# Performance work log

Hardware: AMD Instinct MI355X
Metric: run time of the kernel (lower is better)

## Reference

```python
import jax, jax.numpy as jnp
import numpy as np

D = 128  # inputs / head dim

def setup_inputs() -> dict:
    key = jax.random.key(0)
    ks = jax.random.split(key, 7)
    B, S = 4, 4096
    s = 1.0 / np.sqrt(D)
    return {
        "x": jax.random.normal(ks[0], (B, S, D), dtype=jnp.float32),
        "Wq": jax.random.normal(ks[1], (D, D), dtype=jnp.float32) * s,
        "bq": jax.random.normal(ks[2], (D,), dtype=jnp.float32) * s,
        "Wk": jax.random.normal(ks[3], (D, D), dtype=jnp.float32) * s,
        "bk": jax.random.normal(ks[4], (D,), dtype=jnp.float32) * s,
        "Wv": jax.random.normal(ks[5], (D, D), dtype=jnp.float32) * s,
        "bv": jax.random.normal(ks[6], (D,), dtype=jnp.float32) * s,
    }

def reference(x, Wq, bq, Wk, bk, Wv, bv):
    B, S, d = x.shape
    # nn.Linear: y = x @ W^T + b
    q = jnp.einsum('bsd,ed->bse', x, Wq) + bq
    k = jnp.einsum('bsd,ed->bse', x, Wk) + bk
    v = jnp.einsum('bsd,ed->bse', x, Wv) + bv
    scores = jnp.einsum('bse,bte->bst', q, k) / jnp.sqrt(jnp.asarray(d, x.dtype))
    attn = jax.nn.softmax(scores, axis=-1)
    out = jnp.einsum('bst,bte->bse', attn, v)
    return out.reshape(B, S * d)
```

## Files before the change

kernel.cpp:

```cpp
#include <hip/hip_runtime.h>
#include <hip/hip_bf16.h>

typedef __bf16 bf16x8 __attribute__((ext_vector_type(8)));
typedef __bf16 bf16x4 __attribute__((ext_vector_type(4)));
typedef float  f32x4  __attribute__((ext_vector_type(4)));
typedef _Float16 f16x4 __attribute__((ext_vector_type(4)));

#define NB 4
#define SEQ 4096
#define DIM 128

static __device__ __forceinline__ unsigned int bf16bits(__bf16 h) {
    return (unsigned int)__builtin_bit_cast(unsigned short, h);
}

#define GLOAD_LDS16(g, s) __builtin_amdgcn_global_load_lds(                    \
    (const __attribute__((address_space(1))) void*)(g),                        \
    (__attribute__((address_space(3))) void*)(s), 16, 0, 0)

__global__ __launch_bounds__(256) void wconv(
    const float* __restrict__ Wq, const float* __restrict__ Wk,
    const float* __restrict__ Wv,
    __bf16* __restrict__ Wh, __bf16* __restrict__ Wl)
{
    int idx = blockIdx.x * 256 + threadIdx.x;
    int which = idx >> 12;
    int off = (idx & 4095) * 4;
    const float* W = which == 0 ? Wq : (which == 1 ? Wk : Wv);
    float4 v = *(const float4*)(W + off);
    bf16x4 h, lo;
    h[0] = (__bf16)v.x; h[1] = (__bf16)v.y; h[2] = (__bf16)v.z; h[3] = (__bf16)v.w;
    lo[0] = (__bf16)(v.x - (float)h[0]);
    lo[1] = (__bf16)(v.y - (float)h[1]);
    lo[2] = (__bf16)(v.z - (float)h[2]);
    lo[3] = (__bf16)(v.w - (float)h[3]);
    *(bf16x4*)(Wh + which * 16384 + off) = h;
    *(bf16x4*)(Wl + which * 16384 + off) = lo;
}

union QkvSh {
    float  xs[64][132];
    __bf16 vbuf[64][200];
};

__global__ __launch_bounds__(256) void qkv_proj3(
    const float* __restrict__ x,
    const __bf16* __restrict__ Whg, const __bf16* __restrict__ Wlg,
    const float* __restrict__ bq, const float* __restrict__ bk,
    const float* __restrict__ bv,
    __bf16* __restrict__ Q, __bf16* __restrict__ K, __bf16* __restrict__ Vt)
{
    __shared__ QkvSh sh;
    const int t  = threadIdx.x;
    const int w  = t >> 6, l = t & 63, lg = l >> 4, ll = l & 15;
    const int rt = blockIdx.x;
    const int ct0 = blockIdx.y * 12;

    {
        const float4* xsrc = (const float4*)(x + rt * 64 * 128);
        #pragma unroll
        for (int ii = 0; ii < 8; ++ii) {
            int u = t + ii * 256;
            float4 v4 = xsrc[u];
            *(float4*)&sh.xs[u >> 5][(u & 31) * 4] = v4;
        }
    }
    __syncthreads();

    float bfr[3];
    #pragma unroll
    for (int i = 0; i < 3; ++i) {
        int gct = ct0 + w * 3 + i;
        const float* bias = gct < 8 ? bq : (gct < 16 ? bk : bv);
        bfr[i] = bias[(gct & 7) * 16 + ll];
    }

    f32x4 acc[3][4];
    #pragma unroll
    for (int i = 0; i < 3; ++i)
        #pragma unroll
        for (int rf = 0; rf < 4; ++rf) acc[i][rf] = (f32x4){0.f, 0.f, 0.f, 0.f};

    #pragma unroll 1
    for (int kb = 0; kb < 4; ++kb) {
        bf16x8 xh[4], xl[4];
        #pragma unroll
        for (int rf = 0; rf < 4; ++rf) {
            float4 xa = *(const float4*)&sh.xs[rf * 16 + ll][kb * 32 + lg * 8];
            float4 xb = *(const float4*)&sh.xs[rf * 16 + ll][kb * 32 + lg * 8 + 4];
            float xv[8] = {xa.x, xa.y, xa.z, xa.w, xb.x, xb.y, xb.z, xb.w};
            #pragma unroll
            for (int j = 0; j < 8; ++j) {
                __bf16 h = (__bf16)xv[j];
                xh[rf][j] = h;
                xl[rf][j] = (__bf16)(xv[j] - (float)h);
            }
        }
        #pragma unroll
        for (int i = 0; i < 3; ++i) {
            int gct = ct0 + w * 3 + i;
            const __bf16* wb = Whg + (gct >> 3) * 16384 + ((gct & 7) * 16 + ll) * 128 + kb * 32 + lg * 8;
            const __bf16* lb = Wlg + (gct >> 3) * 16384 + ((gct & 7) * 16 + ll) * 128 + kb * 32 + lg * 8;
            bf16x8 wh = *(const bf16x8*)wb;
            bf16x8 wl = *(const bf16x8*)lb;
            #pragma unroll
            for (int rf = 0; rf < 4; ++rf) {
                acc[i][rf] = __builtin_amdgcn_mfma_f32_16x16x32_bf16(xh[rf], wh, acc[i][rf], 0, 0, 0);
                acc[i][rf] = __builtin_amdgcn_mfma_f32_16x16x32_bf16(xh[rf], wl, acc[i][rf], 0, 0, 0);
                acc[i][rf] = __builtin_amdgcn_mfma_f32_16x16x32_bf16(xl[rf], wh, acc[i][rf], 0, 0, 0);
            }
        }
    }

    __syncthreads();
    const float qscale = 0.08838834764831845f;
    #pragma unroll
    for (int i = 0; i < 3; ++i) {
        int gct = ct0 + w * 3 + i;
        float scale = (gct < 8) ? qscale : 1.0f;
        int lct = w * 3 + i;
        #pragma unroll
        for (int rf = 0; rf < 4; ++rf)
            #pragma unroll
            for (int r = 0; r < 4; ++r)
                sh.vbuf[rf * 16 + lg * 4 + r][lct * 16 + ll] =
                    (__bf16)((acc[i][rf][r] + bfr[i]) * scale);
    }
    __syncthreads();

    #pragma unroll 1
    for (int lct = 0; lct < 12; ++lct) {
        int gct = ct0 + lct;
        if (gct < 16) {
            int row = t >> 2, c = (t & 3) * 4;
            __bf16* base = (gct < 8 ? Q : K);
            bf16x4 v4 = *(const bf16x4*)&sh.vbuf[row][lct * 16 + c];
            *(bf16x4*)(base + (rt * 64 + row) * 128 + (gct & 7) * 16 + c) = v4;
        } else {
            int e = (gct - 16) * 16 + (t >> 4);
            int s0 = (t & 15) * 4;
            int bb = rt >> 6, sb = (rt & 63) * 64 + s0;
            bf16x4 v4;
            #pragma unroll
            for (int j = 0; j < 4; ++j) v4[j] = sh.vbuf[s0 + j][lct * 16 + (t >> 4)];
            *(bf16x4*)(Vt + bb * (128 * 4096) + e * 4096 + sb) = v4;
        }
    }
}

__global__ __launch_bounds__(256, 2) void attn_fwd(
    const __bf16* __restrict__ Qg,
    const __bf16* __restrict__ Kg,
    const __bf16* __restrict__ Vt,
    _Float16* __restrict__ Op, float* __restrict__ m_p, float* __restrict__ l_p,
    int kv_len)
{
    __shared__ __align__(16) __bf16 Kl[2][64][128];
    __shared__ __align__(16) __bf16 Vl[2][128][64];
    __shared__ __align__(16) __bf16 PlT[4][2][16][64];

    const int t  = threadIdx.x;
    const int w  = t >> 6;
    const int l  = t & 63, lg = l >> 4, ll = l & 15;
    const int sK = ll & 7;

    const int nwg = gridDim.x * gridDim.y;
    const int lin = blockIdx.x + gridDim.x * blockIdx.y;
    const int chunk = nwg >> 3;
    const int v = (lin & 7) * chunk + (lin >> 3);
    const int qt = v & 31;
    const int b  = (v >> 5) & 3;
    const int s  = v >> 7;

    const int qrow0 = qt * 128 + w * 32;

    bf16x8 qa[2][4];
    #pragma unroll
    for (int h = 0; h < 2; ++h) {
        const __bf16* qb = Qg + (b * 4096 + qrow0 + h * 16 + ll) * 128 + lg * 8;
        #pragma unroll
        for (int kb = 0; kb < 4; ++kb) qa[h][kb] = *(const bf16x8*)(qb + kb * 32);
    }

    f32x4 o[2][8];
    #pragma unroll
    for (int h = 0; h < 2; ++h)
        #pragma unroll
        for (int dt = 0; dt < 8; ++dt) o[h][dt] = (f32x4){0.f, 0.f, 0.f, 0.f};
    float m[2] = {-1e30f, -1e30f}, lsum[2] = {0.f, 0.f};

    const __bf16* kbase = Kg + ((long)b * 4096 + s * kv_len) * 128;
    const __bf16* vbase = Vt + (long)b * 128 * 4096 + s * kv_len;

    int ksrc_off[4], vsrc_off[4];
    #pragma unroll
    for (int ii = 0; ii < 4; ++ii) {
        int u = w * 256 + ii * 64 + l;
        int kr = u >> 4, kc = u & 15;
        ksrc_off[ii] = kr * 128 + ((kc ^ (kr & 7)) * 8);
        int vr = u >> 3, vc = u & 7;
        vsrc_off[ii] = vr * 4096 + ((vc ^ (vr & 7)) * 8);
    }

    #define STAGE(kv, bp)                                                      \
    do {                                                                       \
        _Pragma("unroll")                                                      \
        for (int ii = 0; ii < 4; ++ii)                                         \
            GLOAD_LDS16(kbase + (long)(kv) * 128 + ksrc_off[ii],               \
                        (char*)&Kl[bp][0][0] + (w * 256 + ii * 64) * 16);      \
        _Pragma("unroll")                                                      \
        for (int ii = 0; ii < 4; ++ii)                                         \
            GLOAD_LDS16(vbase + (kv) + vsrc_off[ii],                           \
                        (char*)&Vl[bp][0][0] + (w * 256 + ii * 64) * 16);      \
    } while (0)

    STAGE(0, 0);
    asm volatile("s_waitcnt vmcnt(0)" ::: "memory");
    __syncthreads();

    const int nit = kv_len >> 6;
    int p = 0;
    for (int it = 0; it < nit; ++it) {
        if (it + 1 < nit) STAGE((it + 1) * 64, p ^ 1);

        f32x4 f[2][4];
        #pragma unroll
        for (int h = 0; h < 2; ++h)
            #pragma unroll
            for (int nt = 0; nt < 4; ++nt) f[h][nt] = (f32x4){0.f, 0.f, 0.f, 0.f};
        #pragma unroll
        for (int nt = 0; nt < 4; ++nt) {
            #pragma unroll
            for (int kb = 0; kb < 4; ++kb) {
                bf16x8 kf = *(const bf16x8*)&Kl[p][nt * 16 + ll][((kb * 4 + lg) ^ sK) * 8];
                f[0][nt] = __builtin_amdgcn_mfma_f32_16x16x32_bf16(kf, qa[0][kb], f[0][nt], 0, 0, 0);
                f[1][nt] = __builtin_amdgcn_mfma_f32_16x16x32_bf16(kf, qa[1][kb], f[1][nt], 0, 0, 0);
            }
        }

        float alpha[2];
        #pragma unroll
        for (int h = 0; h < 2; ++h) {
            float mx = f[h][0][0];
            #pragma unroll
            for (int nt = 0; nt < 4; ++nt)
                #pragma unroll
                for (int r = 0; r < 4; ++r) mx = fmaxf(mx, f[h][nt][r]);
            mx = fmaxf(mx, __shfl_xor(mx, 16, 64));
            mx = fmaxf(mx, __shfl_xor(mx, 32, 64));
            float mnew = fmaxf(m[h], mx);
            alpha[h] = __expf(m[h] - mnew);
            float rsum = 0.f;
            #pragma unroll
            for (int nt = 0; nt < 4; ++nt) {
                __bf16 pb[4];
                #pragma unroll
                for (int r = 0; r < 4; ++r) {
                    float e = __expf(f[h][nt][r] - mnew);
                    pb[r] = (__bf16)e;
                    rsum += (float)pb[r];
                }
                uint2 u2;
                u2.x = bf16bits(pb[0]) | (bf16bits(pb[1]) << 16);
                u2.y = bf16bits(pb[2]) | (bf16bits(pb[3]) << 16);
                *(uint2*)&PlT[w][h][ll][((nt * 4 + lg) ^ (sK << 1)) * 4] = u2;
            }
            rsum += __shfl_xor(rsum, 16, 64);
            rsum += __shfl_xor(rsum, 32, 64);
            lsum[h] = lsum[h] * alpha[h] + rsum;
            m[h] = mnew;
        }
        asm volatile("s_waitcnt lgkmcnt(0)" ::: "memory");
        __builtin_amdgcn_sched_barrier(0);

        #pragma unroll
        for (int h = 0; h < 2; ++h) {
            float arow[4];
            #pragma unroll
            for (int r = 0; r < 4; ++r) arow[r] = __shfl(alpha[h], lg * 4 + r, 64);
            #pragma unroll
            for (int dt = 0; dt < 8; ++dt)
                #pragma unroll
                for (int r = 0; r < 4; ++r) o[h][dt][r] *= arow[r];
        }

        #pragma unroll
        for (int kc = 0; kc < 2; ++kc) {
            bf16x8 pa0 = *(const bf16x8*)&PlT[w][0][ll][((kc * 4 + lg) ^ sK) * 8];
            bf16x8 pa1 = *(const bf16x8*)&PlT[w][1][ll][((kc * 4 + lg) ^ sK) * 8];
            #pragma unroll
            for (int dt = 0; dt < 8; ++dt) {
                bf16x8 vb = *(const bf16x8*)&Vl[p][dt * 16 + ll][((kc * 4 + lg) ^ sK) * 8];
                o[0][dt] = __builtin_amdgcn_mfma_f32_16x16x32_bf16(pa0, vb, o[0][dt], 0, 0, 0);
                o[1][dt] = __builtin_amdgcn_mfma_f32_16x16x32_bf16(pa1, vb, o[1][dt], 0, 0, 0);
            }
        }

        asm volatile("s_waitcnt vmcnt(0)" ::: "memory");
        __syncthreads();
        p ^= 1;
    }
    #undef STAGE

    #pragma unroll
    for (int h = 0; h < 2; ++h) {
        long rowbase = (long)s * (NB * SEQ) + b * 4096 + qrow0 + h * 16;
        _Float16* op = Op + rowbase * 128;
        #pragma unroll
        for (int r = 0; r < 4; ++r)
            #pragma unroll
            for (int dt = 0; dt < 8; ++dt)
                op[(lg * 4 + r) * 128 + dt * 16 + ll] = (_Float16)o[h][dt][r];
        if (lg == 0) {
            m_p[rowbase + ll] = m[h];
            l_p[rowbase + ll] = lsum[h];
        }
    }
}

__global__ __launch_bounds__(256) void attn_merge(
    const _Float16* __restrict__ Op, const float* __restrict__ m_p,
    const float* __restrict__ l_p, float* __restrict__ out, int nsplit)
{
    const int t = threadIdx.x;
    const int base_row = blockIdx.x * 64;
    #pragma unroll 1
    for (int k = 0; k < 8; ++k) {
        int u = t + k * 256;
        int row = base_row + (u >> 5);
        int dq = u & 31;
        float M = -1e30f;
        for (int sp = 0; sp < nsplit; ++sp)
            M = fmaxf(M, m_p[(long)sp * (NB * SEQ) + row]);
        float L = 0.f;
        float4 acc = {0.f, 0.f, 0.f, 0.f};
        for (int sp = 0; sp < nsplit; ++sp) {
            long rb2 = (long)sp * (NB * SEQ) + row;
            float a = __expf(m_p[rb2] - M);
            L += l_p[rb2] * a;
            f16x4 vv = *(const f16x4*)(Op + rb2 * 128 + dq * 4);
            acc.x += (float)vv[0] * a; acc.y += (float)vv[1] * a;
            acc.z += (float)vv[2] * a; acc.w += (float)vv[3] * a;
        }
        float inv = 1.f / L;
        float4 r4 = {acc.x * inv, acc.y * inv, acc.z * inv, acc.w * inv};
        *(float4*)(out + (long)row * 128 + dq * 4) = r4;
    }
}

extern "C" void kernel_launch(void* const* d_in, const int* in_sizes, int n_in,
                              void* d_out, int out_size, void* d_ws, size_t ws_size,
                              hipStream_t stream) {
    (void)in_sizes; (void)n_in; (void)out_size;
    const float* x  = (const float*)d_in[0];
    const float* Wq = (const float*)d_in[1];
    const float* bq = (const float*)d_in[2];
    const float* Wk = (const float*)d_in[3];
    const float* bk = (const float*)d_in[4];
    const float* Wv = (const float*)d_in[5];
    const float* bv = (const float*)d_in[6];
    float* out = (float*)d_out;

    const size_t qkv_elems = (size_t)NB * SEQ * DIM;
    char* p = (char*)d_ws;
    __bf16* Q  = (__bf16*)p;        p += qkv_elems * 2;
    __bf16* K  = (__bf16*)p;        p += qkv_elems * 2;
    __bf16* Vt = (__bf16*)p;        p += qkv_elems * 2;
    __bf16* Wh = (__bf16*)p;        p += 3 * DIM * DIM * 2;
    __bf16* Wl = (__bf16*)p;        p += 3 * DIM * DIM * 2;
    size_t used = (size_t)(p - (char*)d_ws);

    const size_t per_split = (size_t)NB * SEQ * DIM * 2 + 2 * (size_t)NB * SEQ * 4;
    int nsplit = 4;
    while (nsplit > 1 && used + (size_t)nsplit * per_split > ws_size) nsplit >>= 1;

    _Float16* Op = (_Float16*)p;                 p += (size_t)nsplit * NB * SEQ * DIM * 2;
    float* m_p = (float*)p;                      p += (size_t)nsplit * NB * SEQ * 4;
    float* l_p = (float*)p;

    wconv<<<48, 256, 0, stream>>>(Wq, Wk, Wv, Wh, Wl);
    dim3 g1(256, 2);
    qkv_proj3<<<g1, 256, 0, stream>>>(x, Wh, Wl, bq, bk, bv, Q, K, Vt);
    dim3 g2(128, nsplit);
    attn_fwd<<<g2, 256, 0, stream>>>(Q, K, Vt, Op, m_p, l_p, SEQ / nsplit);
    attn_merge<<<256, 256, 0, stream>>>(Op, m_p, l_p, out, nsplit);
}
```

Baseline: 93.43 us.

## Switch attention to 32x32x16 MFMA and keep P in registers via permlane swap

Rewrites the attention inner loop to use 32x32x16 bf16 MFMA tiles, computing S^T so that each lane owns one query row. The softmax probabilities are repacked in registers with v_permlane32_swap instead of going through a per-wave LDS buffer. This removes the LDS round-trip and its waitcnt for P, along with the cross-lane alpha broadcast shuffles, and makes row max and sum reductions cheaper. The trade-offs are larger accumulator register pressure under launch bounds of 2 blocks per CU, and reliance on a gfx950-specific permlane instruction.

```diff
diff --git a/kernel.cpp b/kernel.cpp
--- a/kernel.cpp
+++ b/kernel.cpp
@@ -4,6 +4,7 @@
 typedef __bf16 bf16x8 __attribute__((ext_vector_type(8)));
 typedef __bf16 bf16x4 __attribute__((ext_vector_type(4)));
 typedef float  f32x4  __attribute__((ext_vector_type(4)));
+typedef float  f32x16 __attribute__((ext_vector_type(16)));
 typedef _Float16 f16x4 __attribute__((ext_vector_type(4)));
 
 #define NB 4
@@ -157,12 +158,13 @@
 {
     __shared__ __align__(16) __bf16 Kl[2][64][128];
     __shared__ __align__(16) __bf16 Vl[2][128][64];
-    __shared__ __align__(16) __bf16 PlT[4][2][16][64];
 
     const int t  = threadIdx.x;
     const int w  = t >> 6;
-    const int l  = t & 63, lg = l >> 4, ll = l & 15;
-    const int sK = ll & 7;
+    const int l  = t & 63;
+    const int q  = l & 31;
+    const int hi = l >> 5;
+    const int s8 = l & 7;
 
     const int nwg = gridDim.x * gridDim.y;
     const int lin = blockIdx.x + gridDim.x * blockIdx.y;
@@ -174,20 +176,19 @@
 
     const int qrow0 = qt * 128 + w * 32;
 
-    bf16x8 qa[2][4];
-    #pragma unroll
-    for (int h = 0; h < 2; ++h) {
-        const __bf16* qb = Qg + (b * 4096 + qrow0 + h * 16 + ll) * 128 + lg * 8;
-        #pragma unroll
-        for (int kb = 0; kb < 4; ++kb) qa[h][kb] = *(const bf16x8*)(qb + kb * 32);
-    }
-
-    f32x4 o[2][8];
-    #pragma unroll
-    for (int h = 0; h < 2; ++h)
-        #pragma unroll
-        for (int dt = 0; dt < 8; ++dt) o[h][dt] = (f32x4){0.f, 0.f, 0.f, 0.f};
-    float m[2] = {-1e30f, -1e30f}, lsum[2] = {0.f, 0.f};
+    bf16x8 qf[8];
+    {
+        const __bf16* qb = Qg + ((long)b * 4096 + qrow0 + q) * 128 + hi * 8;
+        #pragma unroll
+        for (int ks = 0; ks < 8; ++ks) qf[ks] = *(const bf16x8*)(qb + ks * 16);
+    }
+
+    f32x16 o32[4];
+    #pragma unroll
+    for (int dblk = 0; dblk < 4; ++dblk)
+        #pragma unroll
+        for (int r = 0; r < 16; ++r) o32[dblk][r] = 0.f;
+    float m = -1e30f, lsum = 0.f;
 
     const __bf16* kbase = Kg + ((long)b * 4096 + s * kv_len) * 128;
     const __bf16* vbase = Vt + (long)b * 128 * 4096 + s * kv_len;
@@ -223,76 +224,68 @@
     for (int it = 0; it < nit; ++it) {
         if (it + 1 < nit) STAGE((it + 1) * 64, p ^ 1);
 
-        f32x4 f[2][4];
-        #pragma unroll
-        for (int h = 0; h < 2; ++h)
-            #pragma unroll
-            for (int nt = 0; nt < 4; ++nt) f[h][nt] = (f32x4){0.f, 0.f, 0.f, 0.f};
-        #pragma unroll
-        for (int nt = 0; nt < 4; ++nt) {
-            #pragma unroll
-            for (int kb = 0; kb < 4; ++kb) {
-                bf16x8 kf = *(const bf16x8*)&Kl[p][nt * 16 + ll][((kb * 4 + lg) ^ sK) * 8];
-                f[0][nt] = __builtin_amdgcn_mfma_f32_16x16x32_bf16(kf, qa[0][kb], f[0][nt], 0, 0, 0);
-                f[1][nt] = __builtin_amdgcn_mfma_f32_16x16x32_bf16(kf, qa[1][kb], f[1][nt], 0, 0, 0);
+        f32x16 f0, f1;
+        #pragma unroll
+        for (int r = 0; r < 16; ++r) { f0[r] = 0.f; f1[r] = 0.f; }
+        #pragma unroll
+        for (int ks = 0; ks < 8; ++ks) {
+            bf16x8 k0 = *(const bf16x8*)&Kl[p][q]     [(((ks * 2 + hi) ^ s8)) * 8];
+            bf16x8 k1 = *(const bf16x8*)&Kl[p][32 + q][(((ks * 2 + hi) ^ s8)) * 8];
+            f0 = __builtin_amdgcn_mfma_f32_32x32x16_bf16(k0, qf[ks], f0, 0, 0, 0);
+            f1 = __builtin_amdgcn_mfma_f32_32x32x16_bf16(k1, qf[ks], f1, 0, 0, 0);
+        }
+
+        float mx = f0[0];
+        #pragma unroll
+        for (int r = 1; r < 16; ++r) mx = fmaxf(mx, f0[r]);
+        #pragma unroll
+        for (int r = 0; r < 16; ++r) mx = fmaxf(mx, f1[r]);
+        mx = fmaxf(mx, __shfl_xor(mx, 32, 64));
+        float mnew = fmaxf(m, mx);
+        float alpha = __expf(m - mnew);
+        m = mnew;
+
+        float rsum = 0.f;
+        unsigned int d0[8], d1[8];
+        #pragma unroll
+        for (int G = 0; G < 8; ++G) {
+            int base = (G & 3) * 4;
+            float pv[4];
+            #pragma unroll
+            for (int c = 0; c < 4; ++c) {
+                float fv = (G >> 2) ? f1[base + c] : f0[base + c];
+                pv[c] = __expf(fv - mnew);
             }
-        }
-
-        float alpha[2];
-        #pragma unroll
-        for (int h = 0; h < 2; ++h) {
-            float mx = f[h][0][0];
-            #pragma unroll
-            for (int nt = 0; nt < 4; ++nt)
-                #pragma unroll
-                for (int r = 0; r < 4; ++r) mx = fmaxf(mx, f[h][nt][r]);
-            mx = fmaxf(mx, __shfl_xor(mx, 16, 64));
-            mx = fmaxf(mx, __shfl_xor(mx, 32, 64));
-            float mnew = fmaxf(m[h], mx);
-            alpha[h] = __expf(m[h] - mnew);
-            float rsum = 0.f;
-            #pragma unroll
-            for (int nt = 0; nt < 4; ++nt) {
-                __bf16 pb[4];
-                #pragma unroll
-                for (int r = 0; r < 4; ++r) {
-                    float e = __expf(f[h][nt][r] - mnew);
-                    pb[r] = (__bf16)e;
-                    rsum += (float)pb[r];
-                }
-                uint2 u2;
-                u2.x = bf16bits(pb[0]) | (bf16bits(pb[1]) << 16);
-                u2.y = bf16bits(pb[2]) | (bf16bits(pb[3]) << 16);
-                *(uint2*)&PlT[w][h][ll][((nt * 4 + lg) ^ (sK << 1)) * 4] = u2;
-            }
-            rsum += __shfl_xor(rsum, 16, 64);
-            rsum += __shfl_xor(rsum, 32, 64);
-            lsum[h] = lsum[h] * alpha[h] + rsum;
-            m[h] = mnew;
-        }
-        asm volatile("s_waitcnt lgkmcnt(0)" ::: "memory");
-        __builtin_amdgcn_sched_barrier(0);
-
-        #pragma unroll
-        for (int h = 0; h < 2; ++h) {
-            float arow[4];
-            #pragma unroll
-            for (int r = 0; r < 4; ++r) arow[r] = __shfl(alpha[h], lg * 4 + r, 64);
-            #pragma unroll
-            for (int dt = 0; dt < 8; ++dt)
-                #pragma unroll
-                for (int r = 0; r < 4; ++r) o[h][dt][r] *= arow[r];
-        }
-
-        #pragma unroll
-        for (int kc = 0; kc < 2; ++kc) {
-            bf16x8 pa0 = *(const bf16x8*)&PlT[w][0][ll][((kc * 4 + lg) ^ sK) * 8];
-            bf16x8 pa1 = *(const bf16x8*)&PlT[w][1][ll][((kc * 4 + lg) ^ sK) * 8];
-            #pragma unroll
-            for (int dt = 0; dt < 8; ++dt) {
-                bf16x8 vb = *(const bf16x8*)&Vl[p][dt * 16 + ll][((kc * 4 + lg) ^ sK) * 8];
-                o[0][dt] = __builtin_amdgcn_mfma_f32_16x16x32_bf16(pa0, vb, o[0][dt], 0, 0, 0);
-                o[1][dt] = __builtin_amdgcn_mfma_f32_16x16x32_bf16(pa1, vb, o[1][dt], 0, 0, 0);
+            __bf16 pb[4];
+            #pragma unroll
+            for (int c = 0; c < 4; ++c) { pb[c] = (__bf16)pv[c]; rsum += (float)pb[c]; }
+            d0[G] = bf16bits(pb[0]) | (bf16bits(pb[1]) << 16);
+            d1[G] = bf16bits(pb[2]) | (bf16bits(pb[3]) << 16);
+        }
+        lsum = lsum * alpha + rsum;
+
+        #pragma unroll
+        for (int dblk = 0; dblk < 4; ++dblk)
+            #pragma unroll
+            for (int r = 0; r < 16; ++r) o32[dblk][r] *= alpha;
+
+        bf16x8 pf[4];
+        #pragma unroll
+        for (int k = 0; k < 4; ++k) {
+            unsigned int a0 = d0[2 * k], b0 = d0[2 * k + 1];
+            unsigned int a1 = d1[2 * k], b1 = d1[2 * k + 1];
+            asm volatile("v_permlane32_swap_b32 %0, %1" : "+v"(a0), "+v"(b0));
+            asm volatile("v_permlane32_swap_b32 %0, %1" : "+v"(a1), "+v"(b1));
+            unsigned int dw[4] = {a0, a1, b0, b1};
+            pf[k] = __builtin_bit_cast(bf16x8, *(uint4*)dw);
+        }
+
+        #pragma unroll
+        for (int k = 0; k < 4; ++k) {
+            #pragma unroll
+            for (int dblk = 0; dblk < 4; ++dblk) {
+                bf16x8 vf = *(const bf16x8*)&Vl[p][dblk * 32 + q][(((k * 2 + hi) ^ s8)) * 8];
+                o32[dblk] = __builtin_amdgcn_mfma_f32_32x32x16_bf16(vf, pf[k], o32[dblk], 0, 0, 0);
             }
         }
 
@@ -302,19 +295,19 @@
     }
     #undef STAGE
 
-    #pragma unroll
-    for (int h = 0; h < 2; ++h) {
-        long rowbase = (long)s * (NB * SEQ) + b * 4096 + qrow0 + h * 16;
-        _Float16* op = Op + rowbase * 128;
-        #pragma unroll
-        for (int r = 0; r < 4; ++r)
-            #pragma unroll
-            for (int dt = 0; dt < 8; ++dt)
-                op[(lg * 4 + r) * 128 + dt * 16 + ll] = (_Float16)o[h][dt][r];
-        if (lg == 0) {
-            m_p[rowbase + ll] = m[h];
-            l_p[rowbase + ll] = lsum[h];
-        }
+    long rowg = (long)s * (NB * SEQ) + b * 4096 + qrow0 + q;
+    _Float16* op = Op + rowg * 128;
+    #pragma unroll
+    for (int dblk = 0; dblk < 4; ++dblk)
+        #pragma unroll
+        for (int d2 = 0; d2 < 4; ++d2)
+            #pragma unroll
+            for (int c = 0; c < 4; ++c)
+                op[dblk * 32 + d2 * 8 + hi * 4 + c] = (_Float16)o32[dblk][d2 * 4 + c];
+    lsum += __shfl_xor(lsum, 32, 64);
+    if (hi == 0) {
+        m_p[rowg] = m;
+        l_p[rowg] = lsum;
     }
 }
 
```

New measurement: 89.32 us, median of 4. 1.05x faster.
